# Kernel optimization log

Hardware: AMD Instinct MI355X
Metric: run time of the kernel (lower is better)

## Reference

```python
import jax, jax.numpy as jnp
import numpy as np

ALPHA = 1.0
NUM_GROUPS = 4  # groups take values in {0,1,2,3}


def setup_inputs() -> dict:
    key = jax.random.key(0)
    k1, k2 = jax.random.split(key)
    B, C = 2000000, 14
    inputs = jax.random.normal(k1, (B, C), dtype=jnp.float32)
    targets = jax.random.randint(k2, (B, C), 0, 2).astype(jnp.float32)
    # fixed group assignment per label (init arg `groups`)
    groups = jnp.array([0, 1, 1, 2, 2, 0, 3, 3, 1, 2, 0, 3, 1, 2], dtype=jnp.int32)
    return {"inputs": inputs, "targets": targets, "groups": groups}


def reference(inputs, targets, groups):
    x, t = inputs, targets
    # BCE with logits, no pos_weight: max(x,0) - x*t + log(1 + exp(-|x|))
    bce = jnp.maximum(x, 0.0) - x * t + jnp.log1p(jnp.exp(-jnp.abs(x)))  # [B, C]
    # per-sample sum of targets within each group: [NUM_GROUPS, B]
    group_sums = jax.ops.segment_sum(t.T, groups, num_segments=NUM_GROUPS)
    # gather each label's group sum back: [C, B]
    gathered = group_sums[groups]
    # group 0 is always kept; other groups kept only if their target sum > 0
    mask = jnp.where(groups[:, None] == 0, 1.0, (gathered > 0).astype(bce.dtype))  # [C, B]
    loss = bce * mask.T * ALPHA  # [B, C]
    return jnp.mean(loss)
```

## Files before the change

### kernel.cpp

```cpp
#include <hip/hip_runtime.h>

#define NCH 14

__device__ __forceinline__ float row_loss(const float* xs, const float* ts, unsigned pack) {
    unsigned gb = 0u;
#pragma unroll
    for (int c = 0; c < NCH; ++c) {
        int gc = (pack >> (2 * c)) & 3;
        gb |= (ts[c] > 0.0f) ? (1u << gc) : 0u;
    }
    float acc = 0.0f;
#pragma unroll
    for (int c = 0; c < NCH; ++c) {
        int gc = (pack >> (2 * c)) & 3;
        float xv = xs[c], tv = ts[c];
        float bce = fmaxf(xv, 0.0f) - xv * tv + __logf(1.0f + __expf(-fabsf(xv)));
        bool keep = (gc == 0) || ((gb >> gc) & 1u);
        acc += keep ? bce : 0.0f;
    }
    return acc;
}

__global__ __launch_bounds__(256) void bce_partial(
    const float* __restrict__ x, const float* __restrict__ t,
    const int* __restrict__ groups, float* __restrict__ partial, int rows)
{
    unsigned pack = 0u;
#pragma unroll
    for (int c = 0; c < NCH; ++c) pack |= ((unsigned)(groups[c] & 3)) << (2 * c);

    const int pairs = rows >> 1;
    const int gtid = blockIdx.x * blockDim.x + threadIdx.x;
    const int nthreads = gridDim.x * blockDim.x;

    float acc = 0.0f;

    for (int p = gtid; p < pairs; p += nthreads) {
        const float4* xp = (const float4*)(x + (size_t)p * (2 * NCH));
        const float4* tp = (const float4*)(t + (size_t)p * (2 * NCH));
        float xs[2 * NCH], ts[2 * NCH];
#pragma unroll
        for (int j = 0; j < 7; ++j) {
            float4 xv = xp[j];
            float4 tv = tp[j];
            xs[4 * j + 0] = xv.x; xs[4 * j + 1] = xv.y; xs[4 * j + 2] = xv.z; xs[4 * j + 3] = xv.w;
            ts[4 * j + 0] = tv.x; ts[4 * j + 1] = tv.y; ts[4 * j + 2] = tv.z; ts[4 * j + 3] = tv.w;
        }
        acc += row_loss(xs, ts, pack);
        acc += row_loss(xs + NCH, ts + NCH, pack);
    }

    if ((rows & 1) && gtid == 0) {
        const size_t base = (size_t)(rows - 1) * NCH;
        float xs[NCH], ts[NCH];
#pragma unroll
        for (int c = 0; c < NCH; ++c) { xs[c] = x[base + c]; ts[c] = t[base + c]; }
        acc += row_loss(xs, ts, pack);
    }

#pragma unroll
    for (int off = 32; off > 0; off >>= 1) acc += __shfl_xor(acc, off);

    __shared__ float wsum[4];
    const int lane = threadIdx.x & 63;
    const int wid = threadIdx.x >> 6;
    if (lane == 0) wsum[wid] = acc;
    __syncthreads();
    if (threadIdx.x == 0)
        partial[blockIdx.x] = wsum[0] + wsum[1] + wsum[2] + wsum[3];
}

__global__ __launch_bounds__(256) void finalize(
    const float* __restrict__ partial, int n, float* __restrict__ out, double inv_count)
{
    double s = 0.0;
    for (int i = threadIdx.x; i < n; i += 256) s += (double)partial[i];

    __shared__ double sd[256];
    sd[threadIdx.x] = s;
    __syncthreads();
#pragma unroll
    for (int step = 128; step > 0; step >>= 1) {
        if (threadIdx.x < step) sd[threadIdx.x] += sd[threadIdx.x + step];
        __syncthreads();
    }
    if (threadIdx.x == 0) out[0] = (float)(sd[0] * inv_count);
}

extern "C" void kernel_launch(void* const* d_in, const int* in_sizes, int n_in,
                              void* d_out, int out_size, void* d_ws, size_t ws_size,
                              hipStream_t stream) {
    const float* x = (const float*)d_in[0];
    const float* t = (const float*)d_in[1];
    const int* groups = (const int*)d_in[2];
    float* out = (float*)d_out;
    float* partial = (float*)d_ws;

    const int total = in_sizes[0];
    const int rows = total / NCH;

    int blocks = 2048;
    if ((size_t)blocks * sizeof(float) > ws_size)
        blocks = (int)(ws_size / sizeof(float));
    if (blocks < 1) blocks = 1;

    bce_partial<<<blocks, 256, 0, stream>>>(x, t, groups, partial, rows);

    const double inv_count = 1.0 / ((double)rows * (double)NCH);
    finalize<<<1, 256, 0, stream>>>(partial, blocks, out, inv_count);
}
```

Before: 43.22 us.

## Stage row tiles through LDS with coalesced float4 loads

Global loads no longer have each thread read its own 112-byte pair of rows, which strides accesses across the wavefront. Each block now copies a 512-row tile of x and t into shared memory with fully coalesced float4 loads, and each thread then reads two rows from LDS. The grid is resized to one block per tile, capped at 8192, so one pass covers the input. This costs 56KB of LDS per block, which limits occupancy, and adds syncthreads per tile. The strided LDS reads may also cause bank conflicts.

Result: slower. 48.44 us (+12.1%).

```diff
diff --git a/kernel.cpp b/kernel.cpp
--- a/kernel.cpp
+++ b/kernel.cpp
@@ -1,8 +1,13 @@
 #include <hip/hip_runtime.h>
 
 #define NCH 14
+#define TR 512
+#define TF (TR * NCH)
+#define TF4 (TF / 4)
+#define BT 256
+#define F4T (TF4 / BT)
 
-__device__ __forceinline__ float row_loss(const float* xs, const float* ts, unsigned pack) {
+__device__ __forceinline__ float row_loss14(const float* xs, const float* ts, unsigned pack) {
     unsigned gb = 0u;
 #pragma unroll
     for (int c = 0; c < NCH; ++c) {
@@ -21,52 +26,77 @@
     return acc;
 }
 
-__global__ __launch_bounds__(256) void bce_partial(
+__global__ __launch_bounds__(BT) void bce_partial(
     const float* __restrict__ x, const float* __restrict__ t,
     const int* __restrict__ groups, float* __restrict__ partial, int rows)
 {
+    __shared__ float sx[TF];
+    __shared__ float st[TF];
+
     unsigned pack = 0u;
 #pragma unroll
     for (int c = 0; c < NCH; ++c) pack |= ((unsigned)(groups[c] & 3)) << (2 * c);
 
-    const int pairs = rows >> 1;
-    const int gtid = blockIdx.x * blockDim.x + threadIdx.x;
-    const int nthreads = gridDim.x * blockDim.x;
-
+    const int tid = threadIdx.x;
+    const int ntiles = (rows + TR - 1) / TR;
     float acc = 0.0f;
 
-    for (int p = gtid; p < pairs; p += nthreads) {
-        const float4* xp = (const float4*)(x + (size_t)p * (2 * NCH));
-        const float4* tp = (const float4*)(t + (size_t)p * (2 * NCH));
-        float xs[2 * NCH], ts[2 * NCH];
+    for (int tile = blockIdx.x; tile < ntiles; tile += gridDim.x) {
+        const size_t base = (size_t)tile * TF;
+        const int tile_rows = min(TR, rows - tile * TR);
+        const int tile_floats = tile_rows * NCH;
+
+        __syncthreads();
+
+        if (tile_floats == TF) {
+            const float4* xg = (const float4*)(x + base);
+            const float4* tg = (const float4*)(t + base);
+            float4 xr[F4T], tr[F4T];
 #pragma unroll
-        for (int j = 0; j < 7; ++j) {
-            float4 xv = xp[j];
-            float4 tv = tp[j];
-            xs[4 * j + 0] = xv.x; xs[4 * j + 1] = xv.y; xs[4 * j + 2] = xv.z; xs[4 * j + 3] = xv.w;
-            ts[4 * j + 0] = tv.x; ts[4 * j + 1] = tv.y; ts[4 * j + 2] = tv.z; ts[4 * j + 3] = tv.w;
+            for (int k = 0; k < F4T; ++k) {
+                xr[k] = xg[k * BT + tid];
+                tr[k] = tg[k * BT + tid];
+            }
+            float4* sxv = (float4*)sx;
+            float4* stv = (float4*)st;
+#pragma unroll
+            for (int k = 0; k < F4T; ++k) {
+                sxv[k * BT + tid] = xr[k];
+                stv[k * BT + tid] = tr[k];
+            }
+        } else {
+            for (int i = tid; i < tile_floats; i += BT) {
+                sx[i] = x[base + i];
+                st[i] = t[base + i];
+            }
         }
-        acc += row_loss(xs, ts, pack);
-        acc += row_loss(xs + NCH, ts + NCH, pack);
-    }
+        __syncthreads();
 
-    if ((rows & 1) && gtid == 0) {
-        const size_t base = (size_t)(rows - 1) * NCH;
-        float xs[NCH], ts[NCH];
+        const int r0 = 2 * tid;
+        if (r0 < tile_rows) {
+            const float4* v = (const float4*)(sx + (size_t)tid * 2 * NCH);
+            const float4* w = (const float4*)(st + (size_t)tid * 2 * NCH);
+            float xs[2 * NCH], ts[2 * NCH];
 #pragma unroll
-        for (int c = 0; c < NCH; ++c) { xs[c] = x[base + c]; ts[c] = t[base + c]; }
-        acc += row_loss(xs, ts, pack);
+            for (int j = 0; j < 7; ++j) {
+                float4 a = v[j], b = w[j];
+                xs[4 * j + 0] = a.x; xs[4 * j + 1] = a.y; xs[4 * j + 2] = a.z; xs[4 * j + 3] = a.w;
+                ts[4 * j + 0] = b.x; ts[4 * j + 1] = b.y; ts[4 * j + 2] = b.z; ts[4 * j + 3] = b.w;
+            }
+            acc += row_loss14(xs, ts, pack);
+            if (r0 + 1 < tile_rows) acc += row_loss14(xs + NCH, ts + NCH, pack);
+        }
     }
 
 #pragma unroll
     for (int off = 32; off > 0; off >>= 1) acc += __shfl_xor(acc, off);
 
-    __shared__ float wsum[4];
-    const int lane = threadIdx.x & 63;
-    const int wid = threadIdx.x >> 6;
+    __shared__ float wsum[BT / 64];
+    const int lane = tid & 63;
+    const int wid = tid >> 6;
     if (lane == 0) wsum[wid] = acc;
     __syncthreads();
-    if (threadIdx.x == 0)
+    if (tid == 0)
         partial[blockIdx.x] = wsum[0] + wsum[1] + wsum[2] + wsum[3];
 }
 
@@ -98,13 +128,15 @@
 
     const int total = in_sizes[0];
     const int rows = total / NCH;
+    const int ntiles = (rows + TR - 1) / TR;
 
-    int blocks = 2048;
+    int blocks = ntiles;
+    if (blocks > 8192) blocks = 8192;
     if ((size_t)blocks * sizeof(float) > ws_size)
         blocks = (int)(ws_size / sizeof(float));
     if (blocks < 1) blocks = 1;
 
-    bce_partial<<<blocks, 256, 0, stream>>>(x, t, groups, partial, rows);
+    bce_partial<<<blocks, BT, 0, stream>>>(x, t, groups, partial, rows);
 
     const double inv_count = 1.0 / ((double)rows * (double)NCH);
     finalize<<<1, 256, 0, stream>>>(partial, blocks, out, inv_count);
```

## Specialize loss kernel for fixed group layout and launch one block per 256 pairs

Applied to the files above, without the earlier changes.

Adds a fast path used when the packed group assignment matches a hardcoded layout. It computes group target sums and masked partial sums with straight-line code instead of per-label bit tricks, and accumulates log2 terms separately so a single multiply by ln2 happens at the end. The grid now uses one block per 256 row pairs, so nearly every thread handles one pair, instead of a fixed 2048-block grid-stride loop. A general fallback path is kept, but the specialization is tied to the test's group layout, and the larger grid produces many more partials for the single-block finalize to sum.

New measurement: 44.94 us. +4.0%, slower.

```diff
diff --git a/kernel.cpp b/kernel.cpp
--- a/kernel.cpp
+++ b/kernel.cpp
@@ -1,67 +1,113 @@
 #include <hip/hip_runtime.h>
 
 #define NCH 14
+#define BT 256
+#define LN2F 0.69314718055994530942f
 
-__device__ __forceinline__ float row_loss(const float* xs, const float* ts, unsigned pack) {
+#define EXPECTED_PACK ((0u<<0)|(1u<<2)|(1u<<4)|(2u<<6)|(2u<<8)|(0u<<10)|(3u<<12)|(3u<<14)| \
+                       (1u<<16)|(2u<<18)|(0u<<20)|(3u<<22)|(1u<<24)|(2u<<26))
+
+__device__ __forceinline__ unsigned make_pack(const int* __restrict__ groups) {
+    unsigned p = 0u;
+#pragma unroll
+    for (int c = 0; c < NCH; ++c) p |= ((unsigned)(groups[c] & 3)) << (2 * c);
+    return p;
+}
+
+__device__ __forceinline__ void row_spec(const float* xs, const float* ts,
+                                         float& accL, float& accG) {
+    float lin[NCH], lg[NCH];
+#pragma unroll
+    for (int c = 0; c < NCH; ++c) {
+        float xv = xs[c];
+        lin[c] = fmaf(-xv, ts[c], fmaxf(xv, 0.0f));
+        float z = __expf(-fabsf(xv));
+        lg[c] = __log2f(1.0f + z);
+    }
+    float s1 = ts[1] + ts[2] + ts[8] + ts[12];
+    float s2 = ts[3] + ts[4] + ts[9] + ts[13];
+    float s3 = ts[6] + ts[7] + ts[11];
+
+    float rL0 = lin[0] + lin[5] + lin[10],            rG0 = lg[0] + lg[5] + lg[10];
+    float rL1 = lin[1] + lin[2] + lin[8] + lin[12],   rG1 = lg[1] + lg[2] + lg[8] + lg[12];
+    float rL2 = lin[3] + lin[4] + lin[9] + lin[13],   rG2 = lg[3] + lg[4] + lg[9] + lg[13];
+    float rL3 = lin[6] + lin[7] + lin[11],            rG3 = lg[6] + lg[7] + lg[11];
+
+    accL += rL0;                        accG += rG0;
+    accL += (s1 > 0.0f) ? rL1 : 0.0f;   accG += (s1 > 0.0f) ? rG1 : 0.0f;
+    accL += (s2 > 0.0f) ? rL2 : 0.0f;   accG += (s2 > 0.0f) ? rG2 : 0.0f;
+    accL += (s3 > 0.0f) ? rL3 : 0.0f;   accG += (s3 > 0.0f) ? rG3 : 0.0f;
+}
+
+__device__ __forceinline__ void row_gen(const float* xs, const float* ts,
+                                        unsigned pack, float& accL, float& accG) {
     unsigned gb = 0u;
 #pragma unroll
     for (int c = 0; c < NCH; ++c) {
         int gc = (pack >> (2 * c)) & 3;
         gb |= (ts[c] > 0.0f) ? (1u << gc) : 0u;
     }
-    float acc = 0.0f;
 #pragma unroll
     for (int c = 0; c < NCH; ++c) {
         int gc = (pack >> (2 * c)) & 3;
-        float xv = xs[c], tv = ts[c];
-        float bce = fmaxf(xv, 0.0f) - xv * tv + __logf(1.0f + __expf(-fabsf(xv)));
+        float xv = xs[c];
+        float lin = fmaf(-xv, ts[c], fmaxf(xv, 0.0f));
+        float lg = __log2f(1.0f + __expf(-fabsf(xv)));
         bool keep = (gc == 0) || ((gb >> gc) & 1u);
-        acc += keep ? bce : 0.0f;
+        accL += keep ? lin : 0.0f;
+        accG += keep ? lg : 0.0f;
     }
-    return acc;
 }
 
-__global__ __launch_bounds__(256) void bce_partial(
+__global__ __launch_bounds__(BT) void bce_partial(
     const float* __restrict__ x, const float* __restrict__ t,
-    const int* __restrict__ groups, float* __restrict__ partial, int rows)
+    const int* __restrict__ groups, float* __restrict__ partial,
+    int rows, int iters)
 {
-    unsigned pack = 0u;
+    const unsigned pack = make_pack(groups);
+    const bool spec = (pack == EXPECTED_PACK);
+    const int pairs = rows >> 1;
+    const int nth = gridDim.x * BT;
+
+    float accL = 0.0f, accG = 0.0f;
+
+    for (int it = 0; it < iters; ++it) {
+        const int p = blockIdx.x * BT + threadIdx.x + it * nth;
+        if (p < pairs) {
+            const float4* xp = (const float4*)(x + (size_t)p * (2 * NCH));
+            const float4* tp = (const float4*)(t + (size_t)p * (2 * NCH));
+            float xs[2 * NCH], ts[2 * NCH];
 #pragma unroll
-    for (int c = 0; c < NCH; ++c) pack |= ((unsigned)(groups[c] & 3)) << (2 * c);
-
-    const int pairs = rows >> 1;
-    const int gtid = blockIdx.x * blockDim.x + threadIdx.x;
-    const int nthreads = gridDim.x * blockDim.x;
-
-    float acc = 0.0f;
-
-    for (int p = gtid; p < pairs; p += nthreads) {
-        const float4* xp = (const float4*)(x + (size_t)p * (2 * NCH));
-        const float4* tp = (const float4*)(t + (size_t)p * (2 * NCH));
-        float xs[2 * NCH], ts[2 * NCH];
-#pragma unroll
-        for (int j = 0; j < 7; ++j) {
-            float4 xv = xp[j];
-            float4 tv = tp[j];
-            xs[4 * j + 0] = xv.x; xs[4 * j + 1] = xv.y; xs[4 * j + 2] = xv.z; xs[4 * j + 3] = xv.w;
-            ts[4 * j + 0] = tv.x; ts[4 * j + 1] = tv.y; ts[4 * j + 2] = tv.z; ts[4 * j + 3] = tv.w;
+            for (int j = 0; j < 7; ++j) {
+                float4 a = xp[j];
+                float4 b = tp[j];
+                xs[4 * j + 0] = a.x; xs[4 * j + 1] = a.y; xs[4 * j + 2] = a.z; xs[4 * j + 3] = a.w;
+                ts[4 * j + 0] = b.x; ts[4 * j + 1] = b.y; ts[4 * j + 2] = b.z; ts[4 * j + 3] = b.w;
+            }
+            if (spec) {
+                row_spec(xs, ts, accL, accG);
+                row_spec(xs + NCH, ts + NCH, accL, accG);
+            } else {
+                row_gen(xs, ts, pack, accL, accG);
+                row_gen(xs + NCH, ts + NCH, pack, accL, accG);
+            }
         }
-        acc += row_loss(xs, ts, pack);
-        acc += row_loss(xs + NCH, ts + NCH, pack);
     }
 
-    if ((rows & 1) && gtid == 0) {
+    if ((rows & 1) && blockIdx.x == 0 && threadIdx.x == 0) {
         const size_t base = (size_t)(rows - 1) * NCH;
         float xs[NCH], ts[NCH];
 #pragma unroll
         for (int c = 0; c < NCH; ++c) { xs[c] = x[base + c]; ts[c] = t[base + c]; }
-        acc += row_loss(xs, ts, pack);
+        row_gen(xs, ts, pack, accL, accG);
     }
+
+    float acc = fmaf(LN2F, accG, accL);
 
 #pragma unroll
     for (int off = 32; off > 0; off >>= 1) acc += __shfl_xor(acc, off);
 
-    __shared__ float wsum[4];
+    __shared__ float wsum[BT / 64];
     const int lane = threadIdx.x & 63;
     const int wid = threadIdx.x >> 6;
     if (lane == 0) wsum[wid] = acc;
@@ -98,13 +144,15 @@
 
     const int total = in_sizes[0];
     const int rows = total / NCH;
+    const int pairs = rows >> 1;
 
-    int blocks = 2048;
+    int blocks = (pairs + BT - 1) / BT;
     if ((size_t)blocks * sizeof(float) > ws_size)
         blocks = (int)(ws_size / sizeof(float));
     if (blocks < 1) blocks = 1;
+    const int iters = (pairs + blocks * BT - 1) / (blocks * BT);
 
-    bce_partial<<<blocks, 256, 0, stream>>>(x, t, groups, partial, rows);
+    bce_partial<<<blocks, BT, 0, stream>>>(x, t, groups, partial, rows, iters);
 
     const double inv_count = 1.0 / ((double)rows * (double)NCH);
     finalize<<<1, 256, 0, stream>>>(partial, blocks, out, inv_count);
```
